# Performance work log

Hardware: AMD Instinct MI355X
Metric: run time of the kernel (lower is better)

## Reference

```python
import jax, jax.numpy as jnp
import numpy as np

N_NODES = 100000
N_EDGES = 1000000
DIM = 64
BN_EPS = 1e-5


def setup_inputs() -> dict:
    key = jax.random.key(0)
    k_x, k_src, k_off, k_w, k_b = jax.random.split(key, 5)
    x = jax.random.normal(k_x, (N_NODES, DIM), dtype=jnp.float32)
    # Build edges with src != dst so add_remaining_self_loops semantics reduce to
    # appending one self-loop per node (no pre-existing self loops).
    src = jax.random.randint(k_src, (N_EDGES,), 0, N_NODES, dtype=jnp.int64)
    off = jax.random.randint(k_off, (N_EDGES,), 1, N_NODES, dtype=jnp.int64)
    dst = (src + off) % N_NODES
    edge_index = jnp.stack([src, dst], axis=0)
    lin_w = jax.random.normal(k_w, (DIM, DIM), dtype=jnp.float32) * (1.0 / np.sqrt(DIM))
    lin_b = jax.random.normal(k_b, (DIM,), dtype=jnp.float32) * 0.01
    bn_gamma = jnp.ones((DIM,), dtype=jnp.float32)
    bn_beta = jnp.zeros((DIM,), dtype=jnp.float32)
    return {"x": x, "edge_index": edge_index, "lin_w": lin_w, "lin_b": lin_b,
            "bn_gamma": bn_gamma, "bn_beta": bn_beta}


def reference(x, edge_index, lin_w, lin_b, bn_gamma, bn_beta):
    N = x.shape[0]
    loops = jnp.arange(N, dtype=edge_index.dtype)
    src = jnp.concatenate([edge_index[0], loops])  # add_remaining_self_loops
    dst = jnp.concatenate([edge_index[1], loops])
    # edge_weight is rebound to None inside MySAGEConv.forward, so message == x_j
    msgs = jnp.take(x, src, axis=0)                      # [E+N, D] gather
    summed = jax.ops.segment_sum(msgs, dst, num_segments=N)
    deg = jax.ops.segment_sum(jnp.ones_like(dst, dtype=x.dtype), dst, num_segments=N)
    aggr = summed / deg[:, None]                         # scatter-mean (deg >= 1)
    out = aggr @ lin_w.T + lin_b                         # linear
    # BatchNorm1d, training mode (batch stats, biased variance)
    mean = out.mean(axis=0)
    var = out.var(axis=0)
    out = (out - mean) * jax.lax.rsqrt(var + BN_EPS) * bn_gamma + bn_beta
    out = out + x                                        # residual (in_dim == out_dim)
    return jax.nn.relu(out)
```

## Files before the change

kernel.cpp:

```cpp
#include <hip/hip_runtime.h>

#define N_NODES 100000
#define N_EDGES 1000000
#define DIM 64
#define BN_EPS 1e-5f

#define CAP 40
#define NSEG 100
#define SEG_NODES 1000
#define SEGCAP 11200
#define BCAP 40
#define EPB 2048
#define NBIN1 489
#define CONV_BLOCKS 3125
#define OVF_CAP 4096
#define GATHER_BLOCKS (N_NODES / 32)

typedef __attribute__((ext_vector_type(8))) short short8_t;
typedef __attribute__((ext_vector_type(4))) float f32x4;

__device__ inline unsigned bf16rne(float f) {
    unsigned u = __float_as_uint(f);
    return (u + 0x7FFFu + ((u >> 16) & 1u)) >> 16;
}
__device__ inline unsigned pack2(float a, float b) {
    return bf16rne(a) | (bf16rne(b) << 16);
}
__device__ inline void unp_add(unsigned d, float& e0, float& e1) {
    e0 += __uint_as_float(d << 16);
    e1 += __uint_as_float(d & 0xFFFF0000u);
}
__device__ inline void add8(float* acc, uint4 v) {
    unp_add(v.x, acc[0], acc[1]);
    unp_add(v.y, acc[2], acc[3]);
    unp_add(v.z, acc[4], acc[5]);
    unp_add(v.w, acc[6], acc[7]);
}

__global__ __launch_bounds__(256) void k_bin1(const int* __restrict__ ei,
                                              const float4* __restrict__ x4,
                                              const float* __restrict__ W,
                                              uint2* __restrict__ seg_buf,
                                              int* __restrict__ seg_cnt,
                                              int* __restrict__ ovf_cnt,
                                              uint2* __restrict__ ovf,
                                              uint4* __restrict__ xh,
                                              unsigned short* __restrict__ Wb) {
    __shared__ int cnt[NSEG];
    __shared__ int base[NSEG];
    __shared__ uint2 pairs[NSEG][BCAP];

    int b = blockIdx.x;
    if (b == NBIN1 + CONV_BLOCKS) {
        for (int t = threadIdx.x; t < DIM * DIM / 2; t += 256) {
            float2 w2 = ((const float2*)W)[t];
            ((unsigned*)Wb)[t] = pack2(w2.x, w2.y);
        }
        return;
    }
    if (b >= NBIN1) {
        int g = (b - NBIN1) * 256 + threadIdx.x;
        float4 lo = x4[2 * g];
        float4 hi = x4[2 * g + 1];
        uint4 r;
        r.x = pack2(lo.x, lo.y);
        r.y = pack2(lo.z, lo.w);
        r.z = pack2(hi.x, hi.y);
        r.w = pack2(hi.z, hi.w);
        xh[8 + g] = r;
        return;
    }

    for (int t = threadIdx.x; t < NSEG; t += 256) cnt[t] = 0;
    __syncthreads();

    const int base4 = b * (EPB / 4);
#pragma unroll
    for (int k = 0; k < 2; ++k) {
        int i4 = base4 + k * 256 + threadIdx.x;
        if (i4 < N_EDGES / 4) {
            int4 s4 = ((const int4*)ei)[i4];
            int4 d4 = ((const int4*)(ei + N_EDGES))[i4];
            int ss[4] = {s4.x, s4.y, s4.z, s4.w};
            int dd[4] = {d4.x, d4.y, d4.z, d4.w};
#pragma unroll
            for (int q = 0; q < 4; ++q) {
                int seg = (unsigned)dd[q] / SEG_NODES;
                int p = atomicAdd(&cnt[seg], 1);
                if (p < BCAP) {
                    pairs[seg][p] = make_uint2((unsigned)ss[q], (unsigned)dd[q]);
                } else {
                    int g = atomicAdd(ovf_cnt, 1);
                    if (g < OVF_CAP) ovf[g] = make_uint2((unsigned)ss[q], (unsigned)dd[q]);
                }
            }
        }
    }
    __syncthreads();

    if (threadIdx.x < NSEG) {
        int c = min(cnt[threadIdx.x], BCAP);
        base[threadIdx.x] = atomicAdd(&seg_cnt[threadIdx.x], c);
    }
    __syncthreads();

    const int wave = threadIdx.x >> 6, lane = threadIdx.x & 63;
    for (int seg = wave; seg < NSEG; seg += 4) {
        int c = min(cnt[seg], BCAP);
        int bs = base[seg];
        for (int i = lane; i < c; i += 64) {
            int pos = bs + i;
            if (pos < SEGCAP) seg_buf[seg * SEGCAP + pos] = pairs[seg][i];
        }
    }
}

__global__ __launch_bounds__(1024) void k_bin2(const uint2* __restrict__ seg_buf,
                                               const int* __restrict__ seg_cnt,
                                               const int* __restrict__ ovf_cnt,
                                               const uint2* __restrict__ ovf,
                                               int* __restrict__ srcs,
                                               int* __restrict__ count) {
    const int s = blockIdx.x;
    __shared__ int lcnt[SEG_NODES];
    for (int t = threadIdx.x; t < SEG_NODES; t += 1024) lcnt[t] = 0;
    __syncthreads();

    int n = seg_cnt[s];
    if (n > SEGCAP) n = SEGCAP;
    const uint2* sb = seg_buf + s * SEGCAP;

    auto place = [&](uint2 pr) {
        int dl = (int)pr.y - s * SEG_NODES;
        int p = atomicAdd(&lcnt[dl], 1);
        if (p < CAP) srcs[(int)pr.y * CAP + p] = (int)pr.x;
    };

    int i = threadIdx.x;
    for (; i + 1024 < n; i += 2048) {
        uint2 a0 = sb[i];
        uint2 a1 = sb[i + 1024];
        place(a0); place(a1);
    }
    for (; i < n; i += 1024) place(sb[i]);

    int oc = *ovf_cnt;
    if (oc > OVF_CAP) oc = OVF_CAP;
    for (int t = threadIdx.x; t < oc; t += 1024) {
        uint2 pr = ovf[t];
        if ((int)((unsigned)pr.y / SEG_NODES) == s) place(pr);
    }
    __syncthreads();

    for (int t = threadIdx.x; t < SEG_NODES; t += 1024)
        count[s * SEG_NODES + t] = lcnt[t];
}

__global__ __launch_bounds__(256) void k_fill_legacy(const int* __restrict__ ei,
                                                     const float4* __restrict__ x4,
                                                     const float* __restrict__ W,
                                                     int* __restrict__ count,
                                                     int* __restrict__ srcs,
                                                     uint4* __restrict__ xh,
                                                     unsigned short* __restrict__ Wb) {
    int b = blockIdx.x;
    if (b == 977 + CONV_BLOCKS) {
        for (int t = threadIdx.x; t < DIM * DIM / 2; t += 256) {
            float2 w2 = ((const float2*)W)[t];
            ((unsigned*)Wb)[t] = pack2(w2.x, w2.y);
        }
        return;
    }
    if (b < 977) {
        int t = b * 256 + threadIdx.x;
        if (t < N_EDGES / 4) {
            int4 s4 = ((const int4*)ei)[t];
            int4 d4 = ((const int4*)(ei + N_EDGES))[t];
            int p0 = atomicAdd(&count[d4.x], 1);
            int p1 = atomicAdd(&count[d4.y], 1);
            int p2 = atomicAdd(&count[d4.z], 1);
            int p3 = atomicAdd(&count[d4.w], 1);
            if (p0 < CAP) srcs[d4.x * CAP + p0] = s4.x;
            if (p1 < CAP) srcs[d4.y * CAP + p1] = s4.y;
            if (p2 < CAP) srcs[d4.z * CAP + p2] = s4.z;
            if (p3 < CAP) srcs[d4.w * CAP + p3] = s4.w;
        }
    } else {
        int g = (b - 977) * 256 + threadIdx.x;
        float4 lo = x4[2 * g];
        float4 hi = x4[2 * g + 1];
        uint4 r;
        r.x = pack2(lo.x, lo.y);
        r.y = pack2(lo.z, lo.w);
        r.z = pack2(hi.x, hi.y);
        r.w = pack2(hi.z, hi.w);
        xh[8 + g] = r;
    }
}

__global__ __launch_bounds__(256) void k_gather_linear(
        const uint4* __restrict__ xh,
        const int* __restrict__ count,
        const int* __restrict__ srcs,
        const unsigned short* __restrict__ Wb,
        const float* __restrict__ bias,
        float* __restrict__ lin_out,
        float* __restrict__ stats8) {
    const int lane = threadIdx.x & 63;
    const int wave = threadIdx.x >> 6;
    const int sub  = lane >> 3;
    const int f8   = lane & 7;

    __shared__ unsigned short ab[32 * 72];
    __shared__ float red0[4][32], red1[4][32];

    const int row = blockIdx.x * 32 + wave * 8 + sub;
    float acc[8] = {0.f, 0.f, 0.f, 0.f, 0.f, 0.f, 0.f, 0.f};
    add8(acc, xh[(row + 1) * 8 + f8]);

    const int ctrue = count[row];
    const int c = (ctrue < CAP) ? ctrue : CAP;
    const int* sp = srcs + row * CAP;
    for (int i = 0; i < c; i += 4) {
        int4 e = *(const int4*)(sp + i);
        int e1 = (i + 1 < c) ? e.y : -1;
        int e2 = (i + 2 < c) ? e.z : -1;
        int e3 = (i + 3 < c) ? e.w : -1;
        uint4 v0 = xh[(e.x + 1) * 8 + f8];
        uint4 v1 = xh[(e1 + 1) * 8 + f8];
        uint4 v2 = xh[(e2 + 1) * 8 + f8];
        uint4 v3 = xh[(e3 + 1) * 8 + f8];
        add8(acc, v0);
        add8(acc, v1);
        add8(acc, v2);
        add8(acc, v3);
    }

    const float inv = 1.0f / (float)(ctrue + 1);
#pragma unroll
    for (int k = 0; k < 8; ++k) acc[k] *= inv;

    uint4 pk;
    pk.x = pack2(acc[0], acc[1]);
    pk.y = pack2(acc[2], acc[3]);
    pk.z = pack2(acc[4], acc[5]);
    pk.w = pack2(acc[6], acc[7]);
    *(uint4*)&ab[(wave * 8 + sub) * 72 + f8 * 8] = pk;
    __syncthreads();

    const int mh = wave & 1, nh = wave >> 1;
    const int m = lane & 15, quad = lane >> 4;

    const unsigned short* ap = &ab[(mh * 16 + m) * 72 + quad * 8];
    short8_t a0 = *(const short8_t*)ap;
    short8_t a1 = *(const short8_t*)(ap + 32);

    const unsigned short* bp0 = Wb + (nh * 32 + m) * 64 + quad * 8;
    short8_t b00 = *(const short8_t*)bp0;
    short8_t b01 = *(const short8_t*)(bp0 + 32);
    const unsigned short* bp1 = bp0 + 16 * 64;
    short8_t b10 = *(const short8_t*)bp1;
    short8_t b11 = *(const short8_t*)(bp1 + 32);

    f32x4 c0 = {0.f, 0.f, 0.f, 0.f}, c1 = {0.f, 0.f, 0.f, 0.f};
    c0 = __builtin_amdgcn_mfma_f32_16x16x32_bf16(a0, b00, c0, 0, 0, 0);
    c0 = __builtin_amdgcn_mfma_f32_16x16x32_bf16(a1, b01, c0, 0, 0, 0);
    c1 = __builtin_amdgcn_mfma_f32_16x16x32_bf16(a0, b10, c1, 0, 0, 0);
    c1 = __builtin_amdgcn_mfma_f32_16x16x32_bf16(a1, b11, c1, 0, 0, 0);

    const int rb = blockIdx.x * 32 + mh * 16 + quad * 4;
#pragma unroll
    for (int f = 0; f < 2; ++f) {
        f32x4 cc = f ? c1 : c0;
        int col = nh * 32 + f * 16 + m;
        float bj = bias[col];
        float q0 = 0.f, q1 = 0.f;
#pragma unroll
        for (int r = 0; r < 4; ++r) {
            float v = cc[r] + bj;
            lin_out[(rb + r) * DIM + col] = v;
            q0 += v;
            q1 += v * v;
        }
        q0 += __shfl_xor(q0, 16); q0 += __shfl_xor(q0, 32);
        q1 += __shfl_xor(q1, 16); q1 += __shfl_xor(q1, 32);
        if (quad == 0) {
            red0[wave][f * 16 + m] = q0;
            red1[wave][f * 16 + m] = q1;
        }
    }
    __syncthreads();
    if (threadIdx.x < DIM) {
        int j = threadIdx.x, jh = j >> 5, jl = j & 31;
        float t0 = red0[2 * jh][jl] + red0[2 * jh + 1][jl];
        float t1 = red1[2 * jh][jl] + red1[2 * jh + 1][jl];
        float* sb = stats8 + (blockIdx.x & 7) * 128;
        atomicAdd(&sb[j], t0);
        atomicAdd(&sb[DIM + j], t1);
    }
}

__global__ __launch_bounds__(256) void k_final(const float4* lin4,
                                               const unsigned short* __restrict__ xh16,
                                               const float* __restrict__ stats8,
                                               const float* __restrict__ gamma,
                                               const float* __restrict__ beta,
                                               float4* out4) {
    __shared__ float ss[2][DIM];
    if (threadIdx.x < DIM) {
        int j = threadIdx.x;
        float s0 = 0.f, s1 = 0.f;
#pragma unroll
        for (int b = 0; b < 8; ++b) {
            s0 += stats8[b * 128 + j];
            s1 += stats8[b * 128 + DIM + j];
        }
        const float invN = 1.0f / (float)N_NODES;
        float mean = s0 * invN;
        float var = s1 * invN - mean * mean;
        float scale = gamma[j] * rsqrtf(var + BN_EPS);
        ss[0][j] = scale;
        ss[1][j] = beta[j] - mean * scale;
    }
    __syncthreads();
    int tid = blockIdx.x * blockDim.x + threadIdx.x;
    int row = tid >> 4;
    int j4 = (tid & 15) * 4;
    float4 l = lin4[tid];
    ushort2 h01 = *(const ushort2*)&xh16[(row + 1) * 64 + j4];
    ushort2 h23 = *(const ushort2*)&xh16[(row + 1) * 64 + j4 + 2];
    float4 o;
    o.x = fmaxf(fmaf(l.x, ss[0][j4 + 0], ss[1][j4 + 0])
                + __uint_as_float((unsigned)h01.x << 16), 0.f);
    o.y = fmaxf(fmaf(l.y, ss[0][j4 + 1], ss[1][j4 + 1])
                + __uint_as_float((unsigned)h01.y << 16), 0.f);
    o.z = fmaxf(fmaf(l.z, ss[0][j4 + 2], ss[1][j4 + 2])
                + __uint_as_float((unsigned)h23.x << 16), 0.f);
    o.w = fmaxf(fmaf(l.w, ss[0][j4 + 3], ss[1][j4 + 3])
                + __uint_as_float((unsigned)h23.y << 16), 0.f);
    out4[tid] = o;
}

extern "C" void kernel_launch(void* const* d_in, const int* in_sizes, int n_in,
                              void* d_out, int out_size, void* d_ws, size_t ws_size,
                              hipStream_t stream) {
    const float* x     = (const float*)d_in[0];
    const int*   ei    = (const int*)d_in[1];
    const float* W     = (const float*)d_in[2];
    const float* bias  = (const float*)d_in[3];
    const float* gamma = (const float*)d_in[4];
    const float* beta  = (const float*)d_in[5];
    float* out = (float*)d_out;

    char* ws = (char*)d_ws;
    float*          stats8  = (float*)(ws);
    int*            seg_cnt = (int*)(ws + 4096);
    int*            ovf_cnt = (int*)(ws + 4608);
    uint2*          ovf     = (uint2*)(ws + 4736);
    uint4*          xh      = (uint4*)(ws + 37504);
    unsigned short* Wb      = (unsigned short*)(ws + 12837632);
    int*            count   = (int*)(ws + 12845824);
    int*            srcs    = (int*)(ws + 13245824);
    uint2*          seg_buf = (uint2*)(ws + 29245824);

    const size_t NEED_BIN = 38205824;

    if (ws_size >= NEED_BIN) {
        hipMemsetAsync(ws, 0, 37632, stream);
        k_bin1<<<NBIN1 + CONV_BLOCKS + 1, 256, 0, stream>>>(
            ei, (const float4*)x, W, seg_buf, seg_cnt, ovf_cnt, ovf, xh, Wb);
        k_bin2<<<NSEG, 1024, 0, stream>>>(seg_buf, seg_cnt, ovf_cnt, ovf,
                                          srcs, count);
    } else {
        hipMemsetAsync(ws, 0, 37632, stream);
        hipMemsetAsync(count, 0, 400000, stream);
        k_fill_legacy<<<977 + CONV_BLOCKS + 1, 256, 0, stream>>>(
            ei, (const float4*)x, W, count, srcs, xh, Wb);
    }

    k_gather_linear<<<GATHER_BLOCKS, 256, 0, stream>>>(
        xh, count, srcs, Wb, bias, out, stats8);

    k_final<<<N_NODES * (DIM / 4) / 256, 256, 0, stream>>>(
        (const float4*)out, (const unsigned short*)xh, stats8, gamma, beta,
        (float4*)out);
}
```

Baseline: 157.7 us.

## Fuse second binning pass into gather kernel via per-block segment scan

Drops the separate per-node CSR fill kernel (k_bin2), its count/srcs global buffers and the legacy fallback path. Each gather block now scans its whole 1024-node destination segment from the packed segment buffer and builds neighbour lists in shared memory for only its own 32 rows. Edge pairs are packed into one 32-bit word (local dst in the high bits, src in the low 17), which halves binning traffic. Segments become power-of-two sized, with more edges per bin1 block and a larger LDS bucket capacity. The trade-off is that each segment buffer is re-read redundantly by 32 blocks, which relies on L2 hits to avoid a launch and a global scatter round trip.

```diff
diff --git a/kernel.cpp b/kernel.cpp
--- a/kernel.cpp
+++ b/kernel.cpp
@@ -6,12 +6,13 @@
 #define BN_EPS 1e-5f
 
 #define CAP 40
-#define NSEG 100
-#define SEG_NODES 1000
-#define SEGCAP 11200
-#define BCAP 40
-#define EPB 2048
-#define NBIN1 489
+#define SEG_SHIFT 10
+#define SEG_NODES 1024
+#define NSEG 98
+#define SEGCAP 11264
+#define BCAP 96
+#define EPB 4096
+#define NBIN1 245
 #define CONV_BLOCKS 3125
 #define OVF_CAP 4096
 #define GATHER_BLOCKS (N_NODES / 32)
@@ -40,7 +41,7 @@
 __global__ __launch_bounds__(256) void k_bin1(const int* __restrict__ ei,
                                               const float4* __restrict__ x4,
                                               const float* __restrict__ W,
-                                              uint2* __restrict__ seg_buf,
+                                              unsigned* __restrict__ seg_buf,
                                               int* __restrict__ seg_cnt,
                                               int* __restrict__ ovf_cnt,
                                               uint2* __restrict__ ovf,
@@ -48,7 +49,7 @@
                                               unsigned short* __restrict__ Wb) {
     __shared__ int cnt[NSEG];
     __shared__ int base[NSEG];
-    __shared__ uint2 pairs[NSEG][BCAP];
+    __shared__ unsigned pairs[NSEG][BCAP];
 
     int b = blockIdx.x;
     if (b == NBIN1 + CONV_BLOCKS) {
@@ -76,7 +77,7 @@
 
     const int base4 = b * (EPB / 4);
 #pragma unroll
-    for (int k = 0; k < 2; ++k) {
+    for (int k = 0; k < 4; ++k) {
         int i4 = base4 + k * 256 + threadIdx.x;
         if (i4 < N_EDGES / 4) {
             int4 s4 = ((const int4*)ei)[i4];
@@ -85,10 +86,12 @@
             int dd[4] = {d4.x, d4.y, d4.z, d4.w};
 #pragma unroll
             for (int q = 0; q < 4; ++q) {
-                int seg = (unsigned)dd[q] / SEG_NODES;
+                int seg = (unsigned)dd[q] >> SEG_SHIFT;
+                unsigned pk = ((unsigned)(dd[q] & (SEG_NODES - 1)) << 17)
+                            | (unsigned)ss[q];
                 int p = atomicAdd(&cnt[seg], 1);
                 if (p < BCAP) {
-                    pairs[seg][p] = make_uint2((unsigned)ss[q], (unsigned)dd[q]);
+                    pairs[seg][p] = pk;
                 } else {
                     int g = atomicAdd(ovf_cnt, 1);
                     if (g < OVF_CAP) ovf[g] = make_uint2((unsigned)ss[q], (unsigned)dd[q]);
@@ -115,112 +118,76 @@
     }
 }
 
-__global__ __launch_bounds__(1024) void k_bin2(const uint2* __restrict__ seg_buf,
-                                               const int* __restrict__ seg_cnt,
-                                               const int* __restrict__ ovf_cnt,
-                                               const uint2* __restrict__ ovf,
-                                               int* __restrict__ srcs,
-                                               int* __restrict__ count) {
-    const int s = blockIdx.x;
-    __shared__ int lcnt[SEG_NODES];
-    for (int t = threadIdx.x; t < SEG_NODES; t += 1024) lcnt[t] = 0;
-    __syncthreads();
-
-    int n = seg_cnt[s];
-    if (n > SEGCAP) n = SEGCAP;
-    const uint2* sb = seg_buf + s * SEGCAP;
-
-    auto place = [&](uint2 pr) {
-        int dl = (int)pr.y - s * SEG_NODES;
-        int p = atomicAdd(&lcnt[dl], 1);
-        if (p < CAP) srcs[(int)pr.y * CAP + p] = (int)pr.x;
-    };
-
-    int i = threadIdx.x;
-    for (; i + 1024 < n; i += 2048) {
-        uint2 a0 = sb[i];
-        uint2 a1 = sb[i + 1024];
-        place(a0); place(a1);
-    }
-    for (; i < n; i += 1024) place(sb[i]);
-
-    int oc = *ovf_cnt;
-    if (oc > OVF_CAP) oc = OVF_CAP;
-    for (int t = threadIdx.x; t < oc; t += 1024) {
-        uint2 pr = ovf[t];
-        if ((int)((unsigned)pr.y / SEG_NODES) == s) place(pr);
-    }
-    __syncthreads();
-
-    for (int t = threadIdx.x; t < SEG_NODES; t += 1024)
-        count[s * SEG_NODES + t] = lcnt[t];
-}
-
-__global__ __launch_bounds__(256) void k_fill_legacy(const int* __restrict__ ei,
-                                                     const float4* __restrict__ x4,
-                                                     const float* __restrict__ W,
-                                                     int* __restrict__ count,
-                                                     int* __restrict__ srcs,
-                                                     uint4* __restrict__ xh,
-                                                     unsigned short* __restrict__ Wb) {
-    int b = blockIdx.x;
-    if (b == 977 + CONV_BLOCKS) {
-        for (int t = threadIdx.x; t < DIM * DIM / 2; t += 256) {
-            float2 w2 = ((const float2*)W)[t];
-            ((unsigned*)Wb)[t] = pack2(w2.x, w2.y);
-        }
-        return;
-    }
-    if (b < 977) {
-        int t = b * 256 + threadIdx.x;
-        if (t < N_EDGES / 4) {
-            int4 s4 = ((const int4*)ei)[t];
-            int4 d4 = ((const int4*)(ei + N_EDGES))[t];
-            int p0 = atomicAdd(&count[d4.x], 1);
-            int p1 = atomicAdd(&count[d4.y], 1);
-            int p2 = atomicAdd(&count[d4.z], 1);
-            int p3 = atomicAdd(&count[d4.w], 1);
-            if (p0 < CAP) srcs[d4.x * CAP + p0] = s4.x;
-            if (p1 < CAP) srcs[d4.y * CAP + p1] = s4.y;
-            if (p2 < CAP) srcs[d4.z * CAP + p2] = s4.z;
-            if (p3 < CAP) srcs[d4.w * CAP + p3] = s4.w;
-        }
-    } else {
-        int g = (b - 977) * 256 + threadIdx.x;
-        float4 lo = x4[2 * g];
-        float4 hi = x4[2 * g + 1];
-        uint4 r;
-        r.x = pack2(lo.x, lo.y);
-        r.y = pack2(lo.z, lo.w);
-        r.z = pack2(hi.x, hi.y);
-        r.w = pack2(hi.z, hi.w);
-        xh[8 + g] = r;
-    }
-}
+struct ScanS { int lcnt[32]; unsigned lists[32][CAP]; };
+struct MmS { unsigned short ab[32 * 72]; float red0[4][32]; float red1[4][32]; };
+union GatherU { ScanS sc; MmS mm; };
 
 __global__ __launch_bounds__(256) void k_gather_linear(
         const uint4* __restrict__ xh,
-        const int* __restrict__ count,
-        const int* __restrict__ srcs,
+        const unsigned* __restrict__ seg_buf,
+        const int* __restrict__ seg_cnt,
+        const int* __restrict__ ovf_cnt,
+        const uint2* __restrict__ ovf,
         const unsigned short* __restrict__ Wb,
         const float* __restrict__ bias,
         float* __restrict__ lin_out,
         float* __restrict__ stats8) {
+    __shared__ GatherU sh;
     const int lane = threadIdx.x & 63;
     const int wave = threadIdx.x >> 6;
-    const int sub  = lane >> 3;
-    const int f8   = lane & 7;
-
-    __shared__ unsigned short ab[32 * 72];
-    __shared__ float red0[4][32], red1[4][32];
-
-    const int row = blockIdx.x * 32 + wave * 8 + sub;
+    const int seg = blockIdx.x >> 5;
+    const int winbase = (blockIdx.x & 31) * 32;
+
+    if (threadIdx.x < 32) sh.sc.lcnt[threadIdx.x] = 0;
+    __syncthreads();
+
+    int n = seg_cnt[seg];
+    if (n > SEGCAP) n = SEGCAP;
+    const unsigned* sb = seg_buf + seg * SEGCAP;
+
+    auto proc = [&](unsigned p) {
+        int wloc = (int)(p >> 17) - winbase;
+        if ((unsigned)wloc < 32u) {
+            int pos = atomicAdd(&sh.sc.lcnt[wloc], 1);
+            if (pos < CAP) sh.sc.lists[wloc][pos] = p & 0x1FFFFu;
+        }
+    };
+
+    for (int i = threadIdx.x * 4; i < n; i += 1024) {
+        uint4 p4;
+        if (i + 4 <= n) {
+            p4 = *(const uint4*)(sb + i);
+        } else {
+            p4.x = sb[i];
+            p4.y = (i + 1 < n) ? sb[i + 1] : 0xFFFFFFFFu;
+            p4.z = (i + 2 < n) ? sb[i + 2] : 0xFFFFFFFFu;
+            p4.w = 0xFFFFFFFFu;
+        }
+        proc(p4.x); proc(p4.y); proc(p4.z); proc(p4.w);
+    }
+    int oc = *ovf_cnt;
+    if (oc > OVF_CAP) oc = OVF_CAP;
+    for (int t = threadIdx.x; t < oc; t += 256) {
+        uint2 pr = ovf[t];
+        if ((int)(pr.y >> SEG_SHIFT) == seg) {
+            int wloc = (int)(pr.y & (SEG_NODES - 1)) - winbase;
+            if ((unsigned)wloc < 32u) {
+                int pos = atomicAdd(&sh.sc.lcnt[wloc], 1);
+                if (pos < CAP) sh.sc.lists[wloc][pos] = pr.x;
+            }
+        }
+    }
+    __syncthreads();
+
+    const int sub = lane >> 3, f8 = lane & 7;
+    const int r = wave * 8 + sub;
+    const int row = blockIdx.x * 32 + r;
     float acc[8] = {0.f, 0.f, 0.f, 0.f, 0.f, 0.f, 0.f, 0.f};
     add8(acc, xh[(row + 1) * 8 + f8]);
 
-    const int ctrue = count[row];
+    const int ctrue = sh.sc.lcnt[r];
     const int c = (ctrue < CAP) ? ctrue : CAP;
-    const int* sp = srcs + row * CAP;
+    const int* sp = (const int*)&sh.sc.lists[r][0];
     for (int i = 0; i < c; i += 4) {
         int4 e = *(const int4*)(sp + i);
         int e1 = (i + 1 < c) ? e.y : -1;
@@ -240,18 +207,20 @@
 #pragma unroll
     for (int k = 0; k < 8; ++k) acc[k] *= inv;
 
+    __syncthreads();
+
     uint4 pk;
     pk.x = pack2(acc[0], acc[1]);
     pk.y = pack2(acc[2], acc[3]);
     pk.z = pack2(acc[4], acc[5]);
     pk.w = pack2(acc[6], acc[7]);
-    *(uint4*)&ab[(wave * 8 + sub) * 72 + f8 * 8] = pk;
+    *(uint4*)&sh.mm.ab[(wave * 8 + sub) * 72 + f8 * 8] = pk;
     __syncthreads();
 
     const int mh = wave & 1, nh = wave >> 1;
     const int m = lane & 15, quad = lane >> 4;
 
-    const unsigned short* ap = &ab[(mh * 16 + m) * 72 + quad * 8];
+    const unsigned short* ap = &sh.mm.ab[(mh * 16 + m) * 72 + quad * 8];
     short8_t a0 = *(const short8_t*)ap;
     short8_t a1 = *(const short8_t*)(ap + 32);
 
@@ -276,27 +245,27 @@
         float bj = bias[col];
         float q0 = 0.f, q1 = 0.f;
 #pragma unroll
-        for (int r = 0; r < 4; ++r) {
-            float v = cc[r] + bj;
-            lin_out[(rb + r) * DIM + col] = v;
+        for (int rr = 0; rr < 4; ++rr) {
+            float v = cc[rr] + bj;
+            lin_out[(rb + rr) * DIM + col] = v;
             q0 += v;
             q1 += v * v;
         }
         q0 += __shfl_xor(q0, 16); q0 += __shfl_xor(q0, 32);
         q1 += __shfl_xor(q1, 16); q1 += __shfl_xor(q1, 32);
         if (quad == 0) {
-            red0[wave][f * 16 + m] = q0;
-            red1[wave][f * 16 + m] = q1;
+            sh.mm.red0[wave][f * 16 + m] = q0;
+            sh.mm.red1[wave][f * 16 + m] = q1;
         }
     }
     __syncthreads();
     if (threadIdx.x < DIM) {
         int j = threadIdx.x, jh = j >> 5, jl = j & 31;
-        float t0 = red0[2 * jh][jl] + red0[2 * jh + 1][jl];
-        float t1 = red1[2 * jh][jl] + red1[2 * jh + 1][jl];
-        float* sb = stats8 + (blockIdx.x & 7) * 128;
-        atomicAdd(&sb[j], t0);
-        atomicAdd(&sb[DIM + j], t1);
+        float t0 = sh.mm.red0[2 * jh][jl] + sh.mm.red0[2 * jh + 1][jl];
+        float t1 = sh.mm.red1[2 * jh][jl] + sh.mm.red1[2 * jh + 1][jl];
+        float* sbk = stats8 + (blockIdx.x & 7) * 128;
+        atomicAdd(&sbk[j], t0);
+        atomicAdd(&sbk[DIM + j], t1);
     }
 }
 
@@ -359,27 +328,15 @@
     uint2*          ovf     = (uint2*)(ws + 4736);
     uint4*          xh      = (uint4*)(ws + 37504);
     unsigned short* Wb      = (unsigned short*)(ws + 12837632);
-    int*            count   = (int*)(ws + 12845824);
-    int*            srcs    = (int*)(ws + 13245824);
-    uint2*          seg_buf = (uint2*)(ws + 29245824);
-
-    const size_t NEED_BIN = 38205824;
-
-    if (ws_size >= NEED_BIN) {
-        hipMemsetAsync(ws, 0, 37632, stream);
-        k_bin1<<<NBIN1 + CONV_BLOCKS + 1, 256, 0, stream>>>(
-            ei, (const float4*)x, W, seg_buf, seg_cnt, ovf_cnt, ovf, xh, Wb);
-        k_bin2<<<NSEG, 1024, 0, stream>>>(seg_buf, seg_cnt, ovf_cnt, ovf,
-                                          srcs, count);
-    } else {
-        hipMemsetAsync(ws, 0, 37632, stream);
-        hipMemsetAsync(count, 0, 400000, stream);
-        k_fill_legacy<<<977 + CONV_BLOCKS + 1, 256, 0, stream>>>(
-            ei, (const float4*)x, W, count, srcs, xh, Wb);
-    }
+    unsigned*       seg_buf = (unsigned*)(ws + 12845824);
+
+    hipMemsetAsync(ws, 0, 37632, stream);
+
+    k_bin1<<<NBIN1 + CONV_BLOCKS + 1, 256, 0, stream>>>(
+        ei, (const float4*)x, W, seg_buf, seg_cnt, ovf_cnt, ovf, xh, Wb);
 
     k_gather_linear<<<GATHER_BLOCKS, 256, 0, stream>>>(
-        xh, count, srcs, Wb, bias, out, stats8);
+        xh, seg_buf, seg_cnt, ovf_cnt, ovf, Wb, bias, out, stats8);
 
     k_final<<<N_NODES * (DIM / 4) / 256, 256, 0, stream>>>(
         (const float4*)out, (const unsigned short*)xh, stats8, gamma, beta,
```

Result: faster. 146.3 us (-7.3%).
